# Kernel tuning notes

Hardware: AMD Instinct MI355X
Metric: run time of the kernel (lower is better)

## Reference

```python
import jax, jax.numpy as jnp
import numpy as np

N, C, T, V, K = 32, 256, 64, 25, 3   # batch, in_channels, frames, joints, adjacency partitions
D = 256                               # out_channels
KT = 9                                # temporal kernel size
PAD = (KT - 1) // 2
EPS = 1e-5                            # BatchNorm eps (torch default)


def setup_inputs() -> dict:
    key = jax.random.key(0)
    ks = jax.random.split(key, 5)
    x = jax.random.normal(ks[0], (N, C, T, V), jnp.float32)
    A = jax.random.uniform(ks[1], (K, V, V), jnp.float32)           # learnable adjacency
    W_gcn = jax.random.normal(ks[2], (K, D, C), jnp.float32) * (2.0 / C) ** 0.5  # K stacked 1x1 convs
    b_gcn = jnp.zeros((K, D), jnp.float32)
    W_tcn = jax.random.normal(ks[3], (D, D, KT, 1), jnp.float32) * (2.0 / (D * KT)) ** 0.5  # kaiming fan_out
    b_tcn = jnp.zeros((D,), jnp.float32)
    gamma = jnp.ones((D,), jnp.float32)   # bn_init(bn, 1)
    beta = jnp.zeros((D,), jnp.float32)
    return dict(x=x, A=A, W_gcn=W_gcn, b_gcn=b_gcn, W_tcn=W_tcn,
                b_tcn=b_tcn, gamma=gamma, beta=beta)


def reference(x, A, W_gcn, b_gcn, W_tcn, b_tcn, gamma, beta):
    # ---- GCN: per-partition 1x1 conv over channels, then graph aggregation via A[k], summed over k ----
    # y[k,n,d,t,v] = sum_c W_gcn[k,d,c] * x[n,c,t,v] + b_gcn[k,d]
    y = jnp.einsum('kdc,nctv->kndtv', W_gcn, x) + b_gcn[:, None, :, None, None]
    # aggregate neighbors: sum_v y[k,n,d,t,v] * A[k,v,w], accumulated over partitions k
    y = jnp.einsum('kndtv,kvw->ndtw', y, A)        # [N, D, T, V]

    # ---- TCN: (9,1) temporal conv + BatchNorm2d (batch statistics) ----
    z = jax.lax.conv_general_dilated(
        y, W_tcn, window_strides=(1, 1), padding=((PAD, PAD), (0, 0)),
        dimension_numbers=('NCHW', 'OIHW', 'NCHW'))
    z = z + b_tcn[None, :, None, None]
    mean = jnp.mean(z, axis=(0, 2, 3), keepdims=True)
    var = jnp.mean((z - mean) ** 2, axis=(0, 2, 3), keepdims=True)  # biased, as torch BN training fwd
    z = gamma[None, :, None, None] * (z - mean) * jax.lax.rsqrt(var + EPS) + beta[None, :, None, None]

    # ---- residual (identity branch: in==out, stride==1) + ReLU ----
    return jax.nn.relu(z + x)
```

## Files before the change

kernel.cpp:

```cpp
#include <hip/hip_runtime.h>
#include <math.h>

typedef unsigned short u16;
typedef short v8s __attribute__((ext_vector_type(8)));
typedef float v4f __attribute__((ext_vector_type(4)));

#define AS1 __attribute__((address_space(1)))
#define AS3 __attribute__((address_space(3)))

__device__ __forceinline__ float bf2f(u16 u) {
    union { unsigned int i; float f; } c; c.i = ((unsigned int)u) << 16; return c.f;
}
__device__ __forceinline__ u16 f2bf(float f) {
    union { float f; unsigned int i; } c; c.f = f;
    unsigned int u = c.i;
    return (u16)((u + 0x7FFFu + ((u >> 16) & 1u)) >> 16);
}
__device__ __forceinline__ void gload_lds16(const void* g, void* l) {
    __builtin_amdgcn_global_load_lds((const AS1 void*)(uintptr_t)g,
                                     (AS3 void*)(unsigned int)(uintptr_t)l,
                                     16, 0, 0);
}

#define Nn 32
#define Tt 64
#define Vv 25
#define NP 51200
#define NBLK 400

__global__ __launch_bounds__(256) void prep_kernel(
    const float* __restrict__ Wg, const float* __restrict__ Wt,
    const float* __restrict__ A, const float* __restrict__ bg,
    u16* __restrict__ Wgb, u16* __restrict__ Wtb,
    float* __restrict__ bias2, float* __restrict__ zpad)
{
    const int idx = blockIdx.x * 256 + threadIdx.x;
    const int stride = gridDim.x * 256;
    for (int i = idx; i < 256 * 2304; i += stride) {
        int d = i / 2304, r = i - d * 2304, dt = r >> 8, c = r & 255;
        Wtb[i] = f2bf(Wt[(d * 256 + c) * 9 + dt]);
    }
    for (int i = idx; i < 256 * 768; i += stride) {
        int d = i / 768, r = i - d * 768, k = r >> 8, c = r & 255;
        Wgb[i] = f2bf(Wg[(k * 256 + d) * 256 + c]);
    }
    for (int i = idx; i < 25 * 256; i += stride) {
        int w = i >> 8, d = i & 255;
        float s = 0.f;
        for (int k = 0; k < 3; ++k) {
            float cs = 0.f;
            for (int v = 0; v < 25; ++v) cs += A[(k * 25 + v) * 25 + w];
            s += bg[k * 256 + d] * cs;
        }
        bias2[i] = s;
    }
    for (int i = idx; i < 256; i += stride) zpad[i] = 0.f;
}

__global__ __launch_bounds__(256) void xa_kernel(
    const float* __restrict__ x, const float* __restrict__ A,
    u16* __restrict__ xa2)
{
    const int t = blockIdx.x, n = blockIdx.y;
    const int tid = threadIdx.x;
    __shared__ float xs[256 * 25];

    for (int i = tid; i < 6400; i += 256) {
        int c = i / 25, v = i - c * 25;
        xs[i] = x[((n * 256 + c) * 64 + t) * 25 + v];
    }
    __syncthreads();

    float xr[25];
    #pragma unroll
    for (int v = 0; v < 25; ++v) xr[v] = xs[tid * 25 + v];

    const size_t pbase = ((size_t)n * 64 + t) * 25;
    #pragma unroll 1
    for (int k = 0; k < 3; ++k) {
        float o[25];
        #pragma unroll
        for (int w = 0; w < 25; ++w) {
            float acc = 0.f;
            #pragma unroll
            for (int v = 0; v < 25; ++v)
                acc = fmaf(xr[v], A[(k * 25 + v) * 25 + w], acc);
            o[w] = acc;
        }
        u16* dst = xa2 + k * 256 + tid;
        #pragma unroll
        for (int w = 0; w < 25; ++w)
            dst[(pbase + w) * 768] = f2bf(o[w]);
    }
}

__global__ __launch_bounds__(512) void gemm1_kernel(
    const u16* __restrict__ Ad, const u16* __restrict__ Bw,
    const float* __restrict__ bias, u16* __restrict__ outB)
{
    __shared__ u16 smem[24576];
    u16* As = smem;
    u16* Bs = smem + 8192;

    const int tid = threadIdx.x;
    const int wid = tid >> 6, lane = tid & 63;
    const int lr = lane & 15, hk = lane >> 4;
    const int wm = wid >> 2, wn = wid & 3;
    const int rA = lane >> 3, sA = lane & 7;

    const int orig = blockIdx.x;
    const int m = (orig & 7) * 50 + (orig >> 3);

    v4f acc[4][4];
    const v4f vzero = {0.f, 0.f, 0.f, 0.f};
    #pragma unroll
    for (int mf = 0; mf < 4; ++mf)
        #pragma unroll
        for (int nf = 0; nf < 4; ++nf) acc[mf][nf] = vzero;

    for (int kt = 0; kt < 12; ++kt) {
        #pragma unroll
        for (int i = 0; i < 2; ++i) {
            const int ch = wid + i * 8;
            const int row = ch * 8 + rA;
            const int ss = sA ^ rA;
            gload_lds16(Ad + (size_t)(m * 128 + row) * 768 + kt * 64 + ss * 8,
                        (char*)As + ch * 1024);
        }
        #pragma unroll
        for (int i = 0; i < 4; ++i) {
            const int ch = wid + i * 8;
            const int d = ch * 8 + rA;
            const int ss = sA ^ rA;
            gload_lds16(Bw + (size_t)d * 768 + kt * 64 + ss * 8,
                        (char*)Bs + ch * 1024);
        }
        __syncthreads();

        v8s a[4][2], b[4][2];
        #pragma unroll
        for (int mf = 0; mf < 4; ++mf)
            #pragma unroll
            for (int kk = 0; kk < 2; ++kk) {
                const int row = wm * 64 + mf * 16 + lr;
                const int slot = kk * 4 + hk;
                a[mf][kk] = *(const v8s*)((const char*)As + row * 128 + ((slot ^ (row & 7)) << 4));
            }
        #pragma unroll
        for (int nf = 0; nf < 4; ++nf)
            #pragma unroll
            for (int kk = 0; kk < 2; ++kk) {
                const int row = wn * 64 + nf * 16 + lr;
                const int slot = kk * 4 + hk;
                b[nf][kk] = *(const v8s*)((const char*)Bs + row * 128 + ((slot ^ (row & 7)) << 4));
            }
        #pragma unroll
        for (int kk = 0; kk < 2; ++kk)
            #pragma unroll
            for (int mf = 0; mf < 4; ++mf)
                #pragma unroll
                for (int nf = 0; nf < 4; ++nf)
                    acc[mf][nf] = __builtin_amdgcn_mfma_f32_16x16x32_bf16(
                        a[mf][kk], b[nf][kk], acc[mf][nf], 0, 0, 0);
        __syncthreads();
    }

    #pragma unroll
    for (int mf = 0; mf < 4; ++mf) {
        #pragma unroll
        for (int j = 0; j < 4; ++j) {
            const int p = m * 128 + wm * 64 + mf * 16 + hk * 4 + j;
            const int w = p % 25;
            #pragma unroll
            for (int nf = 0; nf < 4; ++nf) {
                const int d = wn * 64 + nf * 16 + lr;
                outB[(size_t)p * 256 + d] = f2bf(acc[mf][nf][j] + bias[w * 256 + d]);
            }
        }
    }
}

__global__ __launch_bounds__(512) void tcn_split_kernel(
    const u16* __restrict__ y2T, const u16* __restrict__ Wtb,
    const float* __restrict__ bt, u16* __restrict__ zb1,
    u16* __restrict__ zb2, const u16* __restrict__ zpad)
{
    __shared__ u16 smem[24576];
    u16* As = smem;
    u16* Bs = smem + 8192;

    const int tid = threadIdx.x;
    const int wid = tid >> 6, lane = tid & 63;
    const int lr = lane & 15, hk = lane >> 4;
    const int wm = wid >> 2, wn = wid & 3;
    const int rA = lane >> 3, sA = lane & 7;

    const int orig = blockIdx.x;
    const int swz = (orig & 7) * 100 + (orig >> 3);
    const int split = swz / 400, m = swz % 400;
    const int kt0 = split * 18;
    u16* zbo = split ? zb2 : zb1;

    v4f acc[4][4];
    const v4f vzero = {0.f, 0.f, 0.f, 0.f};
    #pragma unroll
    for (int mf = 0; mf < 4; ++mf)
        #pragma unroll
        for (int nf = 0; nf < 4; ++nf) acc[mf][nf] = vzero;

    for (int kt = kt0; kt < kt0 + 18; ++kt) {
        #pragma unroll
        for (int i = 0; i < 2; ++i) {
            const int ch = wid + i * 8;
            const int row = ch * 8 + rA;
            const int ss = sA ^ rA;
            const int dt = kt >> 2, c0 = (kt & 3) << 6;
            const int p = m * 128 + row;
            const int t = (p % 1600) / 25;
            const int tp = t + dt - 4;
            const u16* srcA = ((unsigned)tp < 64u)
                 ? (y2T + (size_t)(p + (dt - 4) * 25) * 256 + c0 + ss * 8)
                 : zpad;
            gload_lds16(srcA, (char*)As + ch * 1024);
        }
        #pragma unroll
        for (int i = 0; i < 4; ++i) {
            const int ch = wid + i * 8;
            const int d = ch * 8 + rA;
            const int ss = sA ^ rA;
            gload_lds16(Wtb + (size_t)d * 2304 + kt * 64 + ss * 8,
                        (char*)Bs + ch * 1024);
        }
        __syncthreads();

        v8s a[4][2], b[4][2];
        #pragma unroll
        for (int mf = 0; mf < 4; ++mf)
            #pragma unroll
            for (int kk = 0; kk < 2; ++kk) {
                const int row = wm * 64 + mf * 16 + lr;
                const int slot = kk * 4 + hk;
                a[mf][kk] = *(const v8s*)((const char*)As + row * 128 + ((slot ^ (row & 7)) << 4));
            }
        #pragma unroll
        for (int nf = 0; nf < 4; ++nf)
            #pragma unroll
            for (int kk = 0; kk < 2; ++kk) {
                const int row = wn * 64 + nf * 16 + lr;
                const int slot = kk * 4 + hk;
                b[nf][kk] = *(const v8s*)((const char*)Bs + row * 128 + ((slot ^ (row & 7)) << 4));
            }
        #pragma unroll
        for (int kk = 0; kk < 2; ++kk)
            #pragma unroll
            for (int mf = 0; mf < 4; ++mf)
                #pragma unroll
                for (int nf = 0; nf < 4; ++nf)
                    acc[mf][nf] = __builtin_amdgcn_mfma_f32_16x16x32_bf16(
                        a[mf][kk], b[nf][kk], acc[mf][nf], 0, 0, 0);
        __syncthreads();
    }

    #pragma unroll
    for (int nf = 0; nf < 4; ++nf) {
        const int d = wn * 64 + nf * 16 + lr;
        const float bb = split ? 0.f : bt[d];
        #pragma unroll
        for (int mf = 0; mf < 4; ++mf) {
            #pragma unroll
            for (int j = 0; j < 4; ++j) {
                const int p = m * 128 + wm * 64 + mf * 16 + hk * 4 + j;
                zbo[(size_t)p * 256 + d] = f2bf(acc[mf][nf][j] + bb);
            }
        }
    }
}

__global__ __launch_bounds__(256) void zsum_kernel(
    const u16* __restrict__ zb1, const u16* __restrict__ zb2,
    float* __restrict__ psum, float* __restrict__ psq)
{
    const int m = blockIdx.x;
    const int d = threadIdx.x;
    const u16* r1 = zb1 + (size_t)m * 128 * 256 + d;
    const u16* r2 = zb2 + (size_t)m * 128 * 256 + d;
    float s = 0.f, q = 0.f;
    #pragma unroll 4
    for (int r = 0; r < 128; ++r) {
        const float z = bf2f(r1[r * 256]) + bf2f(r2[r * 256]);
        s += z; q += z * z;
    }
    psum[(size_t)d * NBLK + m] = s;
    psq[(size_t)d * NBLK + m]  = q;
}

__global__ __launch_bounds__(256) void bn_stats_kernel(
    const float* __restrict__ psum, const float* __restrict__ psq,
    const float* __restrict__ gamma, const float* __restrict__ beta,
    float* __restrict__ scale, float* __restrict__ shift)
{
    const int d = blockIdx.x, tid = threadIdx.x;
    float s = 0.f, q = 0.f;
    for (int i = tid; i < NBLK; i += 256) {
        s += psum[(size_t)d * NBLK + i];
        q += psq[(size_t)d * NBLK + i];
    }
    #pragma unroll
    for (int off = 32; off; off >>= 1) {
        s += __shfl_down(s, off);
        q += __shfl_down(q, off);
    }
    __shared__ float rs[4], rq[4];
    if ((tid & 63) == 0) { rs[tid >> 6] = s; rq[tid >> 6] = q; }
    __syncthreads();
    if (tid == 0) {
        s = rs[0] + rs[1] + rs[2] + rs[3];
        q = rq[0] + rq[1] + rq[2] + rq[3];
        const float mean = s / 51200.f;
        const float var = q / 51200.f - mean * mean;
        const float inv = rsqrtf(var + 1e-5f);
        scale[d] = gamma[d] * inv;
        shift[d] = beta[d] - gamma[d] * inv * mean;
    }
}

__global__ __launch_bounds__(256) void bn_apply_kernel(
    const u16* __restrict__ zb1, const u16* __restrict__ zb2,
    const float* __restrict__ x, const float* __restrict__ scale,
    const float* __restrict__ shift, float* __restrict__ out)
{
    const int chunk = blockIdx.x;
    const int n = blockIdx.y;
    const int tid = threadIdx.x;
    __shared__ float zs[128 * 66];
    const size_t p0 = (size_t)n * 1600 + chunk * 64;

    for (int half = 0; half < 2; ++half) {
        const int d0 = half * 128;
        if (half) __syncthreads();
        for (int i = tid; i < 128 * 64; i += 256) {
            const int pl = i >> 7, dl = i & 127;
            const size_t idx = (p0 + pl) * 256 + d0 + dl;
            zs[dl * 66 + pl] = bf2f(zb1[idx]) + bf2f(zb2[idx]);
        }
        __syncthreads();
        for (int i = tid; i < 128 * 64; i += 256) {
            const int dl = i >> 6, j = i & 63;
            const int d = d0 + dl;
            const size_t addr = ((size_t)n * 256 + d) * 1600 + chunk * 64 + j;
            const float r = zs[dl * 66 + j] * scale[d] + shift[d] + x[addr];
            out[addr] = fmaxf(r, 0.f);
        }
    }
}

extern "C" void kernel_launch(void* const* d_in, const int* in_sizes, int n_in,
                              void* d_out, int out_size, void* d_ws, size_t ws_size,
                              hipStream_t stream)
{
    const float* x     = (const float*)d_in[0];
    const float* A     = (const float*)d_in[1];
    const float* Wg    = (const float*)d_in[2];
    const float* bg    = (const float*)d_in[3];
    const float* Wt    = (const float*)d_in[4];
    const float* bt    = (const float*)d_in[5];
    const float* gamma = (const float*)d_in[6];
    const float* beta  = (const float*)d_in[7];
    float* out = (float*)d_out;

    char* w = (char*)d_ws;
    u16*   xa2   = (u16*)(w);
    u16*   zb1   = (u16*)(w);
    u16*   y2T   = (u16*)(w + 78643200);
    u16*   zb2   = (u16*)(w + 104857600);
    u16*   Wgb   = (u16*)(w + 131072000);
    u16*   Wtb   = (u16*)(w + 131465216);
    float* bias2 = (float*)(w + 132644864);
    float* psum  = (float*)(w + 132670464);
    float* psq   = (float*)(w + 133080064);
    float* scale = (float*)(w + 133489664);
    float* shift = (float*)(w + 133490688);
    float* zpad  = (float*)(w + 133491712);

    prep_kernel<<<256, 256, 0, stream>>>(Wg, Wt, A, bg, Wgb, Wtb, bias2, zpad);
    xa_kernel<<<dim3(64, 32), 256, 0, stream>>>(x, A, xa2);
    gemm1_kernel<<<NBLK, 512, 0, stream>>>(xa2, Wgb, bias2, y2T);
    tcn_split_kernel<<<800, 512, 0, stream>>>(y2T, Wtb, bt, zb1, zb2,
                                              (const u16*)zpad);
    zsum_kernel<<<NBLK, 256, 0, stream>>>(zb1, zb2, psum, psq);
    bn_stats_kernel<<<256, 256, 0, stream>>>(psum, psq, gamma, beta, scale, shift);
    bn_apply_kernel<<<dim3(25, 32), 256, 0, stream>>>(zb1, zb2, x, scale, shift, out);
}
```

Measured before the change: 200.7 us.

## Split TCN GEMM over output channels and fuse BN partial statistics into epilogue

Replaces the split-K temporal conv GEMM, which wrote two partial bf16 outputs, with a split over output-channel halves that runs the full K=2304 reduction per block. This removes the zsum kernel and the second partial buffer. Per-channel sum and sum-of-squares are now reduced in the GEMM epilogue via shuffles and shared memory. bn_apply then reads a single bf16 buffer. The cost is that A tiles are loaded twice (once per channel half) and blocks use 256 threads with a longer K loop.

```diff
diff --git a/kernel.cpp b/kernel.cpp
--- a/kernel.cpp
+++ b/kernel.cpp
@@ -180,26 +180,26 @@
     }
 }
 
-__global__ __launch_bounds__(512) void tcn_split_kernel(
+__global__ __launch_bounds__(256) void tcn_kernel(
     const u16* __restrict__ y2T, const u16* __restrict__ Wtb,
-    const float* __restrict__ bt, u16* __restrict__ zb1,
-    u16* __restrict__ zb2, const u16* __restrict__ zpad)
-{
-    __shared__ u16 smem[24576];
+    const float* __restrict__ bt, u16* __restrict__ zb,
+    float* __restrict__ psum, float* __restrict__ psq,
+    const u16* __restrict__ zpad)
+{
+    __shared__ u16 smem[16384];
     u16* As = smem;
     u16* Bs = smem + 8192;
 
     const int tid = threadIdx.x;
     const int wid = tid >> 6, lane = tid & 63;
     const int lr = lane & 15, hk = lane >> 4;
-    const int wm = wid >> 2, wn = wid & 3;
+    const int wm = wid >> 1, wn = wid & 1;
     const int rA = lane >> 3, sA = lane & 7;
 
     const int orig = blockIdx.x;
     const int swz = (orig & 7) * 100 + (orig >> 3);
-    const int split = swz / 400, m = swz % 400;
-    const int kt0 = split * 18;
-    u16* zbo = split ? zb2 : zb1;
+    const int nh = swz / 400, m = swz % 400;
+    const int d0 = nh * 128;
 
     v4f acc[4][4];
     const v4f vzero = {0.f, 0.f, 0.f, 0.f};
@@ -208,10 +208,10 @@
         #pragma unroll
         for (int nf = 0; nf < 4; ++nf) acc[mf][nf] = vzero;
 
-    for (int kt = kt0; kt < kt0 + 18; ++kt) {
-        #pragma unroll
-        for (int i = 0; i < 2; ++i) {
-            const int ch = wid + i * 8;
+    for (int kt = 0; kt < 36; ++kt) {
+        #pragma unroll
+        for (int i = 0; i < 4; ++i) {
+            const int ch = wid + i * 4;
             const int row = ch * 8 + rA;
             const int ss = sA ^ rA;
             const int dt = kt >> 2, c0 = (kt & 3) << 6;
@@ -222,13 +222,7 @@
                  ? (y2T + (size_t)(p + (dt - 4) * 25) * 256 + c0 + ss * 8)
                  : zpad;
             gload_lds16(srcA, (char*)As + ch * 1024);
-        }
-        #pragma unroll
-        for (int i = 0; i < 4; ++i) {
-            const int ch = wid + i * 8;
-            const int d = ch * 8 + rA;
-            const int ss = sA ^ rA;
-            gload_lds16(Wtb + (size_t)d * 2304 + kt * 64 + ss * 8,
+            gload_lds16(Wtb + (size_t)(d0 + row) * 2304 + kt * 64 + ss * 8,
                         (char*)Bs + ch * 1024);
         }
         __syncthreads();
@@ -261,37 +255,40 @@
         __syncthreads();
     }
 
+    float s[4], q[4];
     #pragma unroll
     for (int nf = 0; nf < 4; ++nf) {
-        const int d = wn * 64 + nf * 16 + lr;
-        const float bb = split ? 0.f : bt[d];
+        const int d = d0 + wn * 64 + nf * 16 + lr;
+        const float bb = bt[d];
+        s[nf] = 0.f; q[nf] = 0.f;
         #pragma unroll
         for (int mf = 0; mf < 4; ++mf) {
             #pragma unroll
             for (int j = 0; j < 4; ++j) {
                 const int p = m * 128 + wm * 64 + mf * 16 + hk * 4 + j;
-                zbo[(size_t)p * 256 + d] = f2bf(acc[mf][nf][j] + bb);
-            }
-        }
-    }
-}
-
-__global__ __launch_bounds__(256) void zsum_kernel(
-    const u16* __restrict__ zb1, const u16* __restrict__ zb2,
-    float* __restrict__ psum, float* __restrict__ psq)
-{
-    const int m = blockIdx.x;
-    const int d = threadIdx.x;
-    const u16* r1 = zb1 + (size_t)m * 128 * 256 + d;
-    const u16* r2 = zb2 + (size_t)m * 128 * 256 + d;
-    float s = 0.f, q = 0.f;
-    #pragma unroll 4
-    for (int r = 0; r < 128; ++r) {
-        const float z = bf2f(r1[r * 256]) + bf2f(r2[r * 256]);
-        s += z; q += z * z;
-    }
-    psum[(size_t)d * NBLK + m] = s;
-    psq[(size_t)d * NBLK + m]  = q;
+                const float zz = acc[mf][nf][j] + bb;
+                zb[(size_t)p * 256 + d] = f2bf(zz);
+                s[nf] += zz; q[nf] += zz * zz;
+            }
+        }
+        s[nf] += __shfl_xor(s[nf], 16); s[nf] += __shfl_xor(s[nf], 32);
+        q[nf] += __shfl_xor(q[nf], 16); q[nf] += __shfl_xor(q[nf], 32);
+    }
+    __syncthreads();
+    float* red = (float*)smem;
+    if (hk == 0) {
+        #pragma unroll
+        for (int nf = 0; nf < 4; ++nf) {
+            const int dl = wn * 64 + nf * 16 + lr;
+            red[wm * 128 + dl] = s[nf];
+            red[256 + wm * 128 + dl] = q[nf];
+        }
+    }
+    __syncthreads();
+    if (tid < 128) {
+        psum[(size_t)(d0 + tid) * NBLK + m] = red[tid] + red[128 + tid];
+        psq[(size_t)(d0 + tid) * NBLK + m]  = red[256 + tid] + red[384 + tid];
+    }
 }
 
 __global__ __launch_bounds__(256) void bn_stats_kernel(
@@ -325,14 +322,14 @@
 }
 
 __global__ __launch_bounds__(256) void bn_apply_kernel(
-    const u16* __restrict__ zb1, const u16* __restrict__ zb2,
-    const float* __restrict__ x, const float* __restrict__ scale,
-    const float* __restrict__ shift, float* __restrict__ out)
+    const u16* __restrict__ zb, const float* __restrict__ x,
+    const float* __restrict__ scale, const float* __restrict__ shift,
+    float* __restrict__ out)
 {
     const int chunk = blockIdx.x;
     const int n = blockIdx.y;
     const int tid = threadIdx.x;
-    __shared__ float zs[128 * 66];
+    __shared__ u16 zs[128 * 66];
     const size_t p0 = (size_t)n * 1600 + chunk * 64;
 
     for (int half = 0; half < 2; ++half) {
@@ -340,15 +337,14 @@
         if (half) __syncthreads();
         for (int i = tid; i < 128 * 64; i += 256) {
             const int pl = i >> 7, dl = i & 127;
-            const size_t idx = (p0 + pl) * 256 + d0 + dl;
-            zs[dl * 66 + pl] = bf2f(zb1[idx]) + bf2f(zb2[idx]);
+            zs[dl * 66 + pl] = zb[(p0 + pl) * 256 + d0 + dl];
         }
         __syncthreads();
         for (int i = tid; i < 128 * 64; i += 256) {
             const int dl = i >> 6, j = i & 63;
             const int d = d0 + dl;
             const size_t addr = ((size_t)n * 256 + d) * 1600 + chunk * 64 + j;
-            const float r = zs[dl * 66 + j] * scale[d] + shift[d] + x[addr];
+            const float r = bf2f(zs[dl * 66 + j]) * scale[d] + shift[d] + x[addr];
             out[addr] = fmaxf(r, 0.f);
         }
     }
@@ -370,9 +366,8 @@
 
     char* w = (char*)d_ws;
     u16*   xa2   = (u16*)(w);
-    u16*   zb1   = (u16*)(w);
     u16*   y2T   = (u16*)(w + 78643200);
-    u16*   zb2   = (u16*)(w + 104857600);
+    u16*   zb    = (u16*)(w + 104857600);
     u16*   Wgb   = (u16*)(w + 131072000);
     u16*   Wtb   = (u16*)(w + 131465216);
     float* bias2 = (float*)(w + 132644864);
@@ -385,9 +380,8 @@
     prep_kernel<<<256, 256, 0, stream>>>(Wg, Wt, A, bg, Wgb, Wtb, bias2, zpad);
     xa_kernel<<<dim3(64, 32), 256, 0, stream>>>(x, A, xa2);
     gemm1_kernel<<<NBLK, 512, 0, stream>>>(xa2, Wgb, bias2, y2T);
-    tcn_split_kernel<<<800, 512, 0, stream>>>(y2T, Wtb, bt, zb1, zb2,
-                                              (const u16*)zpad);
-    zsum_kernel<<<NBLK, 256, 0, stream>>>(zb1, zb2, psum, psq);
+    tcn_kernel<<<800, 256, 0, stream>>>(y2T, Wtb, bt, zb, psum, psq,
+                                        (const u16*)zpad);
     bn_stats_kernel<<<256, 256, 0, stream>>>(psum, psq, gamma, beta, scale, shift);
-    bn_apply_kernel<<<dim3(25, 32), 256, 0, stream>>>(zb1, zb2, x, scale, shift, out);
-}
+    bn_apply_kernel<<<dim3(25, 32), 256, 0, stream>>>(zb, x, scale, shift, out);
+}
```

New measurement: 199.5 us. No clear change (-0.6%).
